# Optimization experiments

Hardware: AMD Instinct MI355X
Metric: run time of the kernel (lower is better)

The kernel has to match this reference:

```python
import jax, jax.numpy as jnp
import numpy as np

EPS = 1e-8  # torch F.cosine_similarity default eps
N, D, K, S = 200000, 512, 32, 1000

def setup_inputs() -> dict:
    key = jax.random.key(0)
    k1, k2, k3 = jax.random.split(key, 3)
    z = jax.random.normal(k1, (N, D), dtype=jnp.float32)
    knn_neighbors = jax.random.randint(k2, (N, K), 0, N)
    sample_indices = jax.random.randint(k3, (S,), 0, N)
    return {"z": z, "knn_neighbors": knn_neighbors, "sample_indices": sample_indices}

def reference(z, knn_neighbors, sample_indices):
    # Gather sampled centers and their neighbor embeddings.
    centers = z[sample_indices]                         # [S, D]
    neigh = z[knn_neighbors[sample_indices]]            # [S, K, D]
    # Cosine similarity along D (torch semantics: dot / max(|a||b|, eps)).
    dot = jnp.einsum('sd,skd->sk', centers, neigh)      # [S, K]
    norm_c = jnp.linalg.norm(centers, axis=-1)          # [S]
    norm_n = jnp.linalg.norm(neigh, axis=-1)            # [S, K]
    cos = dot / jnp.maximum(norm_c[:, None] * norm_n, EPS)
    # Per-center loss 1 - mean cos sim, averaged over sampled centers.
    return jnp.mean(1.0 - jnp.mean(cos, axis=1))
```

## Files before the change

kernel.cpp:

```cpp
#include <hip/hip_runtime.h>
#include <hip/hip_bf16.h>


#define DDIM 512
#define KNN 32
#define EPSV 1e-8f

__global__ __launch_bounds__(256) void ncl_pair_kernel(
    const float* __restrict__ z,
    const int* __restrict__ knn,
    const int* __restrict__ samp,
    float* __restrict__ block_sums) {
    const int s    = blockIdx.x;
    const int lane = threadIdx.x & 63;
    const int wave = threadIdx.x >> 6;

    const int cidx = samp[s];
    const float4* __restrict__ crow = (const float4*)(z + (size_t)cidx * DDIM);
    const float4 c0 = crow[lane];
    const float4 c1 = crow[64 + lane];

    float cn = c0.x*c0.x + c0.y*c0.y + c0.z*c0.z + c0.w*c0.w
             + c1.x*c1.x + c1.y*c1.y + c1.z*c1.z + c1.w*c1.w;
    #pragma unroll
    for (int off = 32; off; off >>= 1) cn += __shfl_xor(cn, off, 64);
    const float cnorm = sqrtf(cn);

    const int* __restrict__ krow = knn + (size_t)cidx * KNN;

    float wsum = 0.0f;
    #pragma unroll
    for (int kk = 0; kk < KNN / 4; ++kk) {
        const int k    = wave + kk * 4;
        const int nidx = krow[k];
        const float4* __restrict__ nrow = (const float4*)(z + (size_t)nidx * DDIM);
        const float4 n0 = nrow[lane];
        const float4 n1 = nrow[64 + lane];

        float dp = c0.x*n0.x; float nn = n0.x*n0.x;
        dp = fmaf(c0.y, n0.y, dp); nn = fmaf(n0.y, n0.y, nn);
        dp = fmaf(c0.z, n0.z, dp); nn = fmaf(n0.z, n0.z, nn);
        dp = fmaf(c0.w, n0.w, dp); nn = fmaf(n0.w, n0.w, nn);
        dp = fmaf(c1.x, n1.x, dp); nn = fmaf(n1.x, n1.x, nn);
        dp = fmaf(c1.y, n1.y, dp); nn = fmaf(n1.y, n1.y, nn);
        dp = fmaf(c1.z, n1.z, dp); nn = fmaf(n1.z, n1.z, nn);
        dp = fmaf(c1.w, n1.w, dp); nn = fmaf(n1.w, n1.w, nn);

        #pragma unroll
        for (int off = 32; off; off >>= 1) {
            dp += __shfl_xor(dp, off, 64);
            nn += __shfl_xor(nn, off, 64);
        }
        const float denom = fmaxf(cnorm * sqrtf(nn), EPSV);
        wsum += dp / denom;
    }

    __shared__ float red[4];
    if (lane == 0) red[wave] = wsum;
    __syncthreads();
    if (threadIdx.x == 0)
        block_sums[s] = red[0] + red[1] + red[2] + red[3];
}

__global__ __launch_bounds__(256) void ncl_finalize_kernel(
    const float* __restrict__ block_sums, float* __restrict__ out, int S) {
    __shared__ float red[256];
    float acc = 0.0f;
    for (int i = threadIdx.x; i < S; i += 256) acc += block_sums[i];
    red[threadIdx.x] = acc;
    __syncthreads();
    #pragma unroll
    for (int off = 128; off; off >>= 1) {
        if (threadIdx.x < off) red[threadIdx.x] += red[threadIdx.x + off];
        __syncthreads();
    }
    if (threadIdx.x == 0)
        out[0] = 1.0f - red[0] / ((float)S * (float)KNN);
}

extern "C" void kernel_launch(void* const* d_in, const int* in_sizes, int n_in,
                              void* d_out, int out_size, void* d_ws, size_t ws_size,
                              hipStream_t stream) {
    const float* z    = (const float*)d_in[0];
    const int*   knn  = (const int*)d_in[1];
    const int*   samp = (const int*)d_in[2];
    const int    S    = in_sizes[2];

    float* block_sums = (float*)d_ws;
    float* out        = (float*)d_out;

    ncl_pair_kernel<<<S, 256, 0, stream>>>(z, knn, samp, block_sums);
    ncl_finalize_kernel<<<1, 256, 0, stream>>>(block_sums, out, S);
}
```

Measured before the change: 467.9 us.

## Split each sample across eight blocks, one neighbor per wave

The pair kernel now launches eight blocks per sampled center, and each wave handles exactly one neighbor instead of looping over eight. The goal is more independent memory requests in flight for the latency-bound random gathers, since only 1000 blocks ran before. In exchange, each center row is re-read by 32 waves instead of 4, and the finalize kernel reduces eight times more partial sums.

```diff
diff --git a/kernel.cpp b/kernel.cpp
--- a/kernel.cpp
+++ b/kernel.cpp
@@ -11,62 +11,54 @@
     const int* __restrict__ knn,
     const int* __restrict__ samp,
     float* __restrict__ block_sums) {
-    const int s    = blockIdx.x;
+    const int b    = blockIdx.x;
+    const int s    = b >> 3;
+    const int g    = b & 7;
     const int lane = threadIdx.x & 63;
     const int wave = threadIdx.x >> 6;
+    const int k    = g * 4 + wave;
 
     const int cidx = samp[s];
+    const int nidx = knn[(size_t)cidx * KNN + k];
+
     const float4* __restrict__ crow = (const float4*)(z + (size_t)cidx * DDIM);
+    const float4* __restrict__ nrow = (const float4*)(z + (size_t)nidx * DDIM);
     const float4 c0 = crow[lane];
     const float4 c1 = crow[64 + lane];
+    const float4 n0 = nrow[lane];
+    const float4 n1 = nrow[64 + lane];
 
-    float cn = c0.x*c0.x + c0.y*c0.y + c0.z*c0.z + c0.w*c0.w
-             + c1.x*c1.x + c1.y*c1.y + c1.z*c1.z + c1.w*c1.w;
+    float cn = c0.x*c0.x; float dp = c0.x*n0.x; float nn = n0.x*n0.x;
+    cn = fmaf(c0.y, c0.y, cn); dp = fmaf(c0.y, n0.y, dp); nn = fmaf(n0.y, n0.y, nn);
+    cn = fmaf(c0.z, c0.z, cn); dp = fmaf(c0.z, n0.z, dp); nn = fmaf(n0.z, n0.z, nn);
+    cn = fmaf(c0.w, c0.w, cn); dp = fmaf(c0.w, n0.w, dp); nn = fmaf(n0.w, n0.w, nn);
+    cn = fmaf(c1.x, c1.x, cn); dp = fmaf(c1.x, n1.x, dp); nn = fmaf(n1.x, n1.x, nn);
+    cn = fmaf(c1.y, c1.y, cn); dp = fmaf(c1.y, n1.y, dp); nn = fmaf(n1.y, n1.y, nn);
+    cn = fmaf(c1.z, c1.z, cn); dp = fmaf(c1.z, n1.z, dp); nn = fmaf(n1.z, n1.z, nn);
+    cn = fmaf(c1.w, c1.w, cn); dp = fmaf(c1.w, n1.w, dp); nn = fmaf(n1.w, n1.w, nn);
+
     #pragma unroll
-    for (int off = 32; off; off >>= 1) cn += __shfl_xor(cn, off, 64);
-    const float cnorm = sqrtf(cn);
-
-    const int* __restrict__ krow = knn + (size_t)cidx * KNN;
-
-    float wsum = 0.0f;
-    #pragma unroll
-    for (int kk = 0; kk < KNN / 4; ++kk) {
-        const int k    = wave + kk * 4;
-        const int nidx = krow[k];
-        const float4* __restrict__ nrow = (const float4*)(z + (size_t)nidx * DDIM);
-        const float4 n0 = nrow[lane];
-        const float4 n1 = nrow[64 + lane];
-
-        float dp = c0.x*n0.x; float nn = n0.x*n0.x;
-        dp = fmaf(c0.y, n0.y, dp); nn = fmaf(n0.y, n0.y, nn);
-        dp = fmaf(c0.z, n0.z, dp); nn = fmaf(n0.z, n0.z, nn);
-        dp = fmaf(c0.w, n0.w, dp); nn = fmaf(n0.w, n0.w, nn);
-        dp = fmaf(c1.x, n1.x, dp); nn = fmaf(n1.x, n1.x, nn);
-        dp = fmaf(c1.y, n1.y, dp); nn = fmaf(n1.y, n1.y, nn);
-        dp = fmaf(c1.z, n1.z, dp); nn = fmaf(n1.z, n1.z, nn);
-        dp = fmaf(c1.w, n1.w, dp); nn = fmaf(n1.w, n1.w, nn);
-
-        #pragma unroll
-        for (int off = 32; off; off >>= 1) {
-            dp += __shfl_xor(dp, off, 64);
-            nn += __shfl_xor(nn, off, 64);
-        }
-        const float denom = fmaxf(cnorm * sqrtf(nn), EPSV);
-        wsum += dp / denom;
+    for (int off = 32; off; off >>= 1) {
+        cn += __shfl_xor(cn, off, 64);
+        dp += __shfl_xor(dp, off, 64);
+        nn += __shfl_xor(nn, off, 64);
     }
 
     __shared__ float red[4];
-    if (lane == 0) red[wave] = wsum;
+    if (lane == 0) {
+        const float denom = fmaxf(sqrtf(cn) * sqrtf(nn), EPSV);
+        red[wave] = dp / denom;
+    }
     __syncthreads();
     if (threadIdx.x == 0)
-        block_sums[s] = red[0] + red[1] + red[2] + red[3];
+        block_sums[b] = red[0] + red[1] + red[2] + red[3];
 }
 
 __global__ __launch_bounds__(256) void ncl_finalize_kernel(
-    const float* __restrict__ block_sums, float* __restrict__ out, int S) {
+    const float* __restrict__ block_sums, float* __restrict__ out, int nblocks, float inv_sk) {
     __shared__ float red[256];
     float acc = 0.0f;
-    for (int i = threadIdx.x; i < S; i += 256) acc += block_sums[i];
+    for (int i = threadIdx.x; i < nblocks; i += 256) acc += block_sums[i];
     red[threadIdx.x] = acc;
     __syncthreads();
     #pragma unroll
@@ -75,7 +67,7 @@
         __syncthreads();
     }
     if (threadIdx.x == 0)
-        out[0] = 1.0f - red[0] / ((float)S * (float)KNN);
+        out[0] = 1.0f - red[0] * inv_sk;
 }
 
 extern "C" void kernel_launch(void* const* d_in, const int* in_sizes, int n_in,
@@ -85,10 +77,12 @@
     const int*   knn  = (const int*)d_in[1];
     const int*   samp = (const int*)d_in[2];
     const int    S    = in_sizes[2];
+    const int    nblocks = S * 8;
 
     float* block_sums = (float*)d_ws;
     float* out        = (float*)d_out;
 
-    ncl_pair_kernel<<<S, 256, 0, stream>>>(z, knn, samp, block_sums);
-    ncl_finalize_kernel<<<1, 256, 0, stream>>>(block_sums, out, S);
+    ncl_pair_kernel<<<nblocks, 256, 0, stream>>>(z, knn, samp, block_sums);
+    ncl_finalize_kernel<<<1, 256, 0, stream>>>(block_sums, out, nblocks,
+                                               1.0f / ((float)S * (float)KNN));
 }
```

Result: no change. 471.0 us (+0.7%).
